# Optimization experiments

Measured on AMD Instinct MI355X. Metric: run time of the kernel, lower is better.

The kernel has to match this reference:

```python
import jax, jax.numpy as jnp
import numpy as np

N = 100000          # nodes
E = 1600000         # edges
KS = 3              # kernel_size per dim
DIM = 3             # pseudo-coordinate dim
CH = [1, 8, 16, 32, 16, 8, 1]
_BITS = ((0,0,0),(1,0,0),(0,1,0),(1,1,0),(0,0,1),(1,0,1),(0,1,1),(1,1,1))
_STRIDES = (1, KS, KS * KS)


def setup_inputs() -> dict:
    key = jax.random.key(0)
    ks = jax.random.split(key, 32)
    inp = {
        "x": jax.random.normal(ks[0], (N, 1), jnp.float32),
        "edge_index": jax.random.randint(ks[1], (2, E), 0, N),
        "pseudo": jax.random.uniform(ks[2], (E, DIM), dtype=jnp.float32),
    }
    ki = 3
    for i in range(6):
        fi, fo = CH[i], CH[i + 1]
        inp[f"w{i+1}"] = jax.random.normal(ks[ki], (KS**DIM, fi, fo), jnp.float32) / np.float32(np.sqrt(fi * 8)); ki += 1
        inp[f"root{i+1}"] = jax.random.normal(ks[ki], (fi, fo), jnp.float32) / np.float32(np.sqrt(fi)); ki += 1
        inp[f"b{i+1}"] = jnp.zeros((fo,), jnp.float32); ki += 1
    return inp


def spline_conv(x, src, dst, pseudo, W, root, bias):
    """Degree-1 open B-spline SplineConv, sum aggregation (norm=False) + root + bias.
    x: [N,Fin], pseudo: [E,DIM] in [0,1], W: [27,Fin,Fout]."""
    v = pseudo * (KS - 1)                              # [E,DIM] in [0,KS-1]
    f = jnp.clip(jnp.floor(v), 0.0, KS - 2)           # left knot per dim
    frac = v - f                                       # fractional part
    fi = f.astype(jnp.int32)
    # transform every node by all 27 kernel matrices once: [N,27,Fout]
    xw = jnp.einsum('nf,kfo->nko', x, W)
    m = jnp.zeros((src.shape[0], W.shape[-1]), x.dtype)
    for bits in _BITS:                                 # 2^DIM = 8 nonzero basis fns
        w = jnp.ones((src.shape[0],), x.dtype)
        idx = jnp.zeros((src.shape[0],), jnp.int32)
        for d in range(DIM):
            w = w * (frac[:, d] if bits[d] else (1.0 - frac[:, d]))
            idx = idx + (fi[:, d] + bits[d]) * _STRIDES[d]
        m = m + w[:, None] * xw[src, idx]              # gather [E,Fout]
    out = jax.ops.segment_sum(m, dst, num_segments=x.shape[0])
    return out + x @ root + bias


def reference(x, edge_index, pseudo, w1, root1, b1, w2, root2, b2, w3, root3, b3,
              w4, root4, b4, w5, root5, b5, w6, root6, b6):
    src, dst = edge_index[0], edge_index[1]
    h = x
    for (W, R, B) in ((w1, root1, b1), (w2, root2, b2), (w3, root3, b3),
                      (w4, root4, b4), (w5, root5, b5), (w6, root6, b6)):
        h = jax.nn.elu(spline_conv(h, src, dst, pseudo, W, R, B))
    return h.reshape(-1)
```

## Files before the change

kernel.cpp:

```cpp
#include <hip/hip_runtime.h>
#include <hip/hip_fp16.h>

#define N_NODES 100000
#define N_EDGES 1600000
#define TS      1024
#define NTILE   ((N_NODES + TS - 1) / TS)
#define NGRP    (NTILE * 8)
#define E_PAD2  (N_EDGES + NGRP * 64 + 256)
#define GRID_E2 (E_PAD2 / 256)

typedef _Float16 f16x8 __attribute__((ext_vector_type(8)));
typedef float    f32x4 __attribute__((ext_vector_type(4)));


__device__ __forceinline__ void pseudo_to_of(float p0, float p1, float p2,
                                             int& oct, float& fr0, float& fr1, float& fr2) {
    float v0 = p0 * 2.0f, v1 = p1 * 2.0f, v2 = p2 * 2.0f;
    int i0 = v0 >= 1.0f, i1 = v1 >= 1.0f, i2 = v2 >= 1.0f;
    fr0 = v0 - (float)i0; fr1 = v1 - (float)i1; fr2 = v2 - (float)i2;
    oct = i0 + 2 * i1 + 4 * i2;
}

template<int Fin>
__device__ __forceinline__ void loadx(const float* __restrict__ hp, float* x) {
    if constexpr (Fin % 4 == 0) {
        const float4* xv = reinterpret_cast<const float4*>(hp);
        #pragma unroll
        for (int f = 0; f < Fin / 4; ++f) {
            float4 t = xv[f];
            x[4*f+0] = t.x; x[4*f+1] = t.y; x[4*f+2] = t.z; x[4*f+3] = t.w;
        }
    } else {
        #pragma unroll
        for (int f = 0; f < Fin; ++f) x[f] = hp[f];
    }
}

template<int CH>
__device__ __forceinline__ void store_m_f16(__half* __restrict__ p, const float* z) {
    if constexpr (CH % 8 == 0) {
        #pragma unroll
        for (int q = 0; q < CH / 8; ++q) {
            union { uint4 v; __half2 h2[4]; } u;
            #pragma unroll
            for (int r = 0; r < 4; ++r)
                u.h2[r] = __floats2half2_rn(z[q*8 + 2*r], z[q*8 + 2*r + 1]);
            ((uint4*)p)[q] = u.v;
        }
    } else if constexpr (CH % 2 == 0) {
        #pragma unroll
        for (int q = 0; q < CH / 2; ++q)
            ((__half2*)p)[q] = __floats2half2_rn(z[2*q], z[2*q+1]);
    } else {
        #pragma unroll
        for (int o = 0; o < CH; ++o) p[o] = __float2half(z[o]);
    }
}

template<int CH>
__device__ __forceinline__ void accum_m_f16(float* acc, const __half* __restrict__ p) {
    if constexpr (CH % 8 == 0) {
        #pragma unroll
        for (int q = 0; q < CH / 8; ++q) {
            union { uint4 v; __half2 h2[4]; } u;
            u.v = ((const uint4*)p)[q];
            #pragma unroll
            for (int r = 0; r < 4; ++r) {
                float2 f = __half22float2(u.h2[r]);
                acc[q*8 + 2*r]     += f.x;
                acc[q*8 + 2*r + 1] += f.y;
            }
        }
    } else if constexpr (CH % 2 == 0) {
        #pragma unroll
        for (int q = 0; q < CH / 2; ++q) {
            float2 f = __half22float2(((const __half2*)p)[q]);
            acc[2*q] += f.x; acc[2*q+1] += f.y;
        }
    } else {
        #pragma unroll
        for (int o = 0; o < CH; ++o) acc[o] += __half2float(p[o]);
    }
}


__global__ __launch_bounds__(256) void count8_k(const int* __restrict__ dst,
                                                const float* __restrict__ pseudo,
                                                int* __restrict__ cnt8,
                                                unsigned short* __restrict__ rank16) {
    int e = blockIdx.x * 256 + threadIdx.x;
    if (e >= N_EDGES) return;
    int d = dst[e];
    size_t pb = (size_t)e * 3;
    int oct; float a, b, c;
    pseudo_to_of(pseudo[pb], pseudo[pb + 1], pseudo[pb + 2], oct, a, b, c);
    int r = atomicAdd(&cnt8[d * 8 + oct], 1);
    rank16[e] = (unsigned short)r;
}

__global__ __launch_bounds__(256) void scan_g1(const int* __restrict__ cnt8,
                                               int* __restrict__ gsum) {
    __shared__ int red[256];
    int g = blockIdx.x, t = threadIdx.x;
    int tile = g >> 3, oct = g & 7;
    int s = 0;
    #pragma unroll
    for (int q = 0; q < 4; ++q) {
        int n = tile * TS + t * 4 + q;
        if (n < N_NODES) s += cnt8[n * 8 + oct];
    }
    red[t] = s;
    __syncthreads();
    #pragma unroll
    for (int off = 128; off > 0; off >>= 1) {
        if (t < off) red[t] += red[t + off];
        __syncthreads();
    }
    if (t == 0) gsum[g] = red[0];
}

__global__ __launch_bounds__(1024) void scan_g2(const int* __restrict__ gsum,
                                                int* __restrict__ gbase,
                                                int* __restrict__ tot,
                                                unsigned char* __restrict__ winoct,
                                                uint4* __restrict__ slotmeta) {
    __shared__ int s[1024];
    __shared__ int sraw;
    int t = threadIdx.x;
    int v = 0;
    if (t < NGRP) v = ((gsum[t] + 63) >> 6) << 6;
    s[t] = v;
    __syncthreads();
    #pragma unroll
    for (int off = 1; off < 1024; off <<= 1) {
        int u = (t >= off) ? s[t - off] : 0;
        __syncthreads();
        s[t] += u;
        __syncthreads();
    }
    if (t < NGRP) gbase[t] = s[t] - v;
    if (t == NGRP - 1) sraw = s[t];
    __syncthreads();
    int raw = sraw;
    int totp = (raw + 255) & ~255;
    if (t == 0) { tot[0] = raw; tot[1] = totp; }
    int fill = totp - raw;
    if (t < fill) {
        uint4 z; z.x = z.y = z.z = z.w = 0u;
        slotmeta[raw + t] = z;
    }
    if (t < (fill >> 6)) winoct[(raw >> 6) + t] = 0;
}

__global__ __launch_bounds__(256) void scan_g3(const int* __restrict__ cnt8,
                                               const int* __restrict__ gbase,
                                               int* __restrict__ slotstart,
                                               unsigned char* __restrict__ winoct,
                                               uint4* __restrict__ slotmeta) {
    __shared__ int s[256];
    int g = blockIdx.x, t = threadIdx.x;
    int tile = g >> 3, oct = g & 7;
    int c[4];
    int sum = 0;
    #pragma unroll
    for (int q = 0; q < 4; ++q) {
        int n = tile * TS + t * 4 + q;
        c[q] = (n < N_NODES) ? cnt8[n * 8 + oct] : 0;
        sum += c[q];
    }
    s[t] = sum;
    __syncthreads();
    #pragma unroll
    for (int off = 1; off < 256; off <<= 1) {
        int u = (t >= off) ? s[t - off] : 0;
        __syncthreads();
        s[t] += u;
        __syncthreads();
    }
    int base = gbase[g];
    int run = base + s[t] - sum;
    #pragma unroll
    for (int q = 0; q < 4; ++q) {
        int n = tile * TS + t * 4 + q;
        if (n < N_NODES) { slotstart[n * 8 + oct] = run; run += c[q]; }
    }
    int cntg = s[255];
    int padded = ((cntg + 63) >> 6) << 6;
    for (int w = t; w < (padded >> 6); w += 256)
        winoct[(base >> 6) + w] = (unsigned char)oct;
    for (int i = t; i < padded - cntg; i += 256) {
        uint4 z; z.x = z.y = z.z = z.w = 0u;
        slotmeta[base + cntg + i] = z;
    }
}

__global__ __launch_bounds__(256) void scatter2_k(const int* __restrict__ src,
                                                  const int* __restrict__ dst,
                                                  const float* __restrict__ pseudo,
                                                  const unsigned short* __restrict__ rank16,
                                                  const int* __restrict__ slotstart,
                                                  uint4* __restrict__ slotmeta) {
    int e = blockIdx.x * 256 + threadIdx.x;
    if (e >= N_EDGES) return;
    int d = dst[e];
    size_t pb = (size_t)e * 3;
    int oct; float fr0, fr1, fr2;
    pseudo_to_of(pseudo[pb], pseudo[pb + 1], pseudo[pb + 2], oct, fr0, fr1, fr2);
    int slot = slotstart[d * 8 + oct] + (int)rank16[e];
    union { uint4 v; struct { int s; __half2 f01; __half2 f2x; unsigned pad; } t; } su;
    su.t.s   = src[e];
    su.t.f01 = __floats2half2_rn(fr0, fr1);
    su.t.f2x = __floats2half2_rn(fr2, 0.0f);
    su.t.pad = 0u;
    slotmeta[slot] = su.v;
}


template<int Fin, int Fout>
__global__ __launch_bounds__(256) void wprep_k(const float* __restrict__ W,
                                               _Float16* __restrict__ WB) {
    constexpr int K  = 8 * Fin;
    constexpr int KT = K / 32;
    constexpr int NT = (Fout + 15) / 16;
    const int total = 8 * KT * NT * 64 * 8;
    int i = blockIdx.x * 256 + threadIdx.x;
    if (i >= total) return;
    int j    = i & 7;
    int lane = (i >> 3) & 63;
    int rest = i >> 9;
    int nt = rest % NT; rest /= NT;
    int kt = rest % KT;
    int g  = rest / KT;
    int kb = lane >> 4, n = lane & 15;
    int k  = kt * 32 + kb * 8 + j;
    int b  = k / Fin, f = k % Fin;
    int bidx = (g & 1) + 3 * ((g >> 1) & 1) + 9 * ((g >> 2) & 1);
    int idx  = bidx + (b & 1) + 3 * ((b >> 1) & 1) + 9 * ((b >> 2) & 1);
    int col  = nt * 16 + n;
    float v = (col < Fout) ? W[((size_t)idx * Fin + f) * Fout + col] : 0.0f;
    WB[i] = (_Float16)v;
}


template<int Fin, int Fout>
__global__ __launch_bounds__(256) void msg_mfma_k(const float* __restrict__ h,
                                                  const uint4* __restrict__ slotmeta,
                                                  const unsigned char* __restrict__ winoct,
                                                  const int* __restrict__ tot,
                                                  const _Float16* __restrict__ WB,
                                                  __half* __restrict__ m) {
    constexpr int K  = 8 * Fin;
    constexpr int KT = K / 32;
    constexpr int NT = (Fout + 15) / 16;
    constexpr int LOG2FIN = (Fin == 8) ? 3 : (Fin == 16) ? 4 : 5;
    constexpr int XR = Fin;
    constexpr int ZR = NT * 16 + 8;

    __shared__ __align__(16) _Float16 xbuf[4][64 * XR];
    __shared__ __align__(16) _Float16 wbuf[4][64 * 8];
    __shared__ __align__(16) _Float16 zbuf[4][64 * ZR];

    const int base = blockIdx.x * 256;
    if (base >= tot[1]) return;

    const int tid = threadIdx.x, wv = tid >> 6, lane = tid & 63;
    const int slot = base + tid;

    int oct = winoct[(base >> 6) + wv];
    oct = __builtin_amdgcn_readfirstlane(oct);

    union { uint4 v; struct { int s; __half2 f01; __half2 f2x; unsigned pad; } t; } u;
    u.v = slotmeta[slot];
    int s = u.t.s;
    float2 f01 = __half22float2(u.t.f01);
    float2 f2x = __half22float2(u.t.f2x);
    float fr0 = f01.x, fr1 = f01.y, fr2 = f2x.x;
    float a0[2] = {1.0f - fr0, fr0};
    float a1[2] = {1.0f - fr1, fr1};
    float a2[2] = {1.0f - fr2, fr2};
    {
        union { uint4 v; __half2 h2[4]; } wu;
        #pragma unroll
        for (int q = 0; q < 4; ++q) {
            float wlo = a0[(2*q) & 1]     * a1[((2*q) >> 1) & 1]     * a2[((2*q) >> 2) & 1];
            float whi = a0[(2*q+1) & 1]   * a1[((2*q+1) >> 1) & 1]   * a2[((2*q+1) >> 2) & 1];
            wu.h2[q] = __floats2half2_rn(wlo, whi);
        }
        *((uint4*)&wbuf[wv][lane * 8]) = wu.v;
    }
    {
        float x[Fin];
        loadx<Fin>(h + (size_t)s * Fin, x);
        union { uint4 v[(Fin + 7) / 8]; __half2 h2[Fin / 2]; } xu;
        #pragma unroll
        for (int f = 0; f < Fin / 2; ++f)
            xu.h2[f] = __floats2half2_rn(x[2*f], x[2*f+1]);
        #pragma unroll
        for (int r = 0; r < Fin / 8; ++r)
            ((uint4*)&xbuf[wv][lane * XR])[r] = xu.v[r];
    }
    __syncthreads();

    f32x4 acc[4][NT];
    #pragma unroll
    for (int mt = 0; mt < 4; ++mt)
        #pragma unroll
        for (int nt = 0; nt < NT; ++nt)
            acc[mt][nt] = (f32x4){0.0f, 0.0f, 0.0f, 0.0f};

    const int kb = lane >> 4;
    const f16x8* __restrict__ WBv = (const f16x8*)WB;

    #pragma unroll
    for (int kt = 0; kt < KT; ++kt) {
        f16x8 bf[NT];
        #pragma unroll
        for (int nt = 0; nt < NT; ++nt)
            bf[nt] = WBv[((oct * KT + kt) * NT + nt) * 64 + lane];

        const int k0 = kt * 32 + kb * 8;
        const int b  = k0 >> LOG2FIN;
        const int f0 = k0 & (Fin - 1);

        #pragma unroll
        for (int mt = 0; mt < 4; ++mt) {
            const int e = mt * 16 + (lane & 15);
            f16x8 xa = *(const f16x8*)&xbuf[wv][e * XR + f0];
            _Float16 wh = wbuf[wv][e * 8 + b];
            f16x8 av;
            #pragma unroll
            for (int j = 0; j < 8; ++j) av[j] = xa[j] * wh;
            #pragma unroll
            for (int nt = 0; nt < NT; ++nt)
                acc[mt][nt] = __builtin_amdgcn_mfma_f32_16x16x32_f16(av, bf[nt], acc[mt][nt], 0, 0, 0);
        }
    }

    #pragma unroll
    for (int mt = 0; mt < 4; ++mt) {
        #pragma unroll
        for (int nt = 0; nt < NT; ++nt) {
            #pragma unroll
            for (int q = 0; q < 4; ++q) {
                int e = mt * 16 + (lane >> 4) * 4 + q;
                int o = nt * 16 + (lane & 15);
                zbuf[wv][e * ZR + o] = (_Float16)acc[mt][nt][q];
            }
        }
    }
    __syncthreads();

    constexpr int NV = (Fout * 2) / 16;
    const uint4* zr = (const uint4*)&zbuf[wv][lane * ZR];
    uint4* mp = (uint4*)(m + (size_t)slot * Fout);
    #pragma unroll
    for (int r = 0; r < NV; ++r) mp[r] = zr[r];
}


template<int Fin, int Fout, int CH>
__global__ __launch_bounds__(256) void msg_k(const float* __restrict__ h,
                                             const uint4* __restrict__ slotmeta,
                                             const unsigned char* __restrict__ winoct,
                                             const int* __restrict__ tot,
                                             const float* __restrict__ W,
                                             __half* __restrict__ m,
                                             int coff) {
    int base = blockIdx.x * 256;
    if (base >= tot[1]) return;
    int wv = threadIdx.x >> 6;
    int g = winoct[(base >> 6) + wv];
    g = __builtin_amdgcn_readfirstlane(g);
    const int bidx = (g & 1) + 3 * ((g >> 1) & 1) + 9 * ((g >> 2) & 1);

    int j = base + threadIdx.x;

    union { uint4 v; struct { int s; __half2 f01; __half2 f2x; unsigned pad; } t; } u;
    u.v = slotmeta[j];
    int s = u.t.s;
    float2 f01 = __half22float2(u.t.f01);
    float2 f2x = __half22float2(u.t.f2x);
    float fr0 = f01.x, fr1 = f01.y, fr2 = f2x.x;
    float a0[2] = {1.0f - fr0, fr0};
    float a1[2] = {1.0f - fr1, fr1};
    float a2[2] = {1.0f - fr2, fr2};
    float w[8];
    #pragma unroll
    for (int b = 0; b < 8; ++b)
        w[b] = a0[b & 1] * a1[(b >> 1) & 1] * a2[(b >> 2) & 1];

    float x[Fin];
    loadx<Fin>(h + (size_t)s * Fin, x);

    float z[CH];
    #pragma unroll
    for (int o = 0; o < CH; ++o) z[o] = 0.0f;

    #pragma unroll
    for (int b = 0; b < 8; ++b) {
        const int idx = bidx + (b & 1) + 3 * ((b >> 1) & 1) + 9 * ((b >> 2) & 1);
        const float* __restrict__ wp = W + (size_t)idx * (Fin * Fout) + coff;
        float wb = w[b];
        #pragma unroll
        for (int f = 0; f < Fin; ++f) {
            float a = wb * x[f];
            #pragma unroll
            for (int o = 0; o < CH; ++o) z[o] = fmaf(a, wp[f * Fout + o], z[o]);
        }
    }

    store_m_f16<CH>(m + (size_t)j * CH, z);
}


template<int Fin, int Fout, int CH>
__global__ __launch_bounds__(256) void gather_k(const float* __restrict__ hin,
                                                const __half* __restrict__ m,
                                                const int* __restrict__ slotstart,
                                                const int* __restrict__ cnt8,
                                                const float* __restrict__ root,
                                                const float* __restrict__ bias,
                                                float* __restrict__ hout,
                                                int coff) {
    int n = blockIdx.x * 256 + threadIdx.x;
    if (n >= N_NODES) return;

    float acc[CH];
    #pragma unroll
    for (int o = 0; o < CH; ++o) acc[o] = bias[coff + o];

    float x[Fin];
    loadx<Fin>(hin + (size_t)n * Fin, x);
    #pragma unroll
    for (int f = 0; f < Fin; ++f) {
        #pragma unroll
        for (int o = 0; o < CH; ++o)
            acc[o] = fmaf(x[f], root[f * Fout + coff + o], acc[o]);
    }

    int4 sa = ((const int4*)slotstart)[n * 2];
    int4 sb = ((const int4*)slotstart)[n * 2 + 1];
    int4 ca = ((const int4*)cnt8)[n * 2];
    int4 cb = ((const int4*)cnt8)[n * 2 + 1];
    int ss[8] = {sa.x, sa.y, sa.z, sa.w, sb.x, sb.y, sb.z, sb.w};
    int cc[8] = {ca.x, ca.y, ca.z, ca.w, cb.x, cb.y, cb.z, cb.w};

    #pragma unroll
    for (int oct = 0; oct < 8; ++oct) {
        int p = ss[oct];
        for (int j = 0; j < cc[oct]; ++j)
            accum_m_f16<CH>(acc, m + (size_t)(p + j) * CH);
    }

    #pragma unroll
    for (int o = 0; o < CH; ++o) {
        float t = acc[o];
        hout[(size_t)n * Fout + coff + o] = t > 0.0f ? t : expm1f(t);
    }
}


template<int Fin, int Fout>
__global__ __launch_bounds__(256) void init_out_k(const float* __restrict__ h,
                                                  const float* __restrict__ root,
                                                  const float* __restrict__ bias,
                                                  float* __restrict__ out) {
    int n = blockIdx.x * 256 + threadIdx.x;
    if (n >= N_NODES) return;
    float xr[Fin];
    #pragma unroll
    for (int f = 0; f < Fin; ++f) xr[f] = h[(size_t)n * Fin + f];
    float z[Fout];
    #pragma unroll
    for (int o = 0; o < Fout; ++o) z[o] = bias[o];
    #pragma unroll
    for (int f = 0; f < Fin; ++f)
        #pragma unroll
        for (int o = 0; o < Fout; ++o) z[o] += xr[f] * root[f * Fout + o];
    #pragma unroll
    for (int o = 0; o < Fout; ++o) out[(size_t)n * Fout + o] = z[o];
}

template<int Fin, int Fout>
__global__ __launch_bounds__(256) void edge_k(const float* __restrict__ h,
                                              const int* __restrict__ src,
                                              const int* __restrict__ dst,
                                              const float* __restrict__ pseudo,
                                              const float* __restrict__ W,
                                              float* __restrict__ out) {
    constexpr int KFF = Fin * Fout;
    constexpr int STRIDE = KFF + 1;
    __shared__ float sW[27 * STRIDE];
    for (int i = threadIdx.x; i < 27 * KFF; i += 256) {
        int k = i / KFF;
        sW[k * STRIDE + (i - k * KFF)] = W[i];
    }
    __syncthreads();
    int e = blockIdx.x * 256 + threadIdx.x;
    if (e >= N_EDGES) return;
    int s = src[e], d = dst[e];
    size_t pb = (size_t)e * 3;
    int oct; float fr0, fr1, fr2;
    pseudo_to_of(pseudo[pb], pseudo[pb+1], pseudo[pb+2], oct, fr0, fr1, fr2);
    int i0 = oct & 1, i1 = (oct >> 1) & 1, i2 = (oct >> 2) & 1;
    float a0[2] = {1.0f - fr0, fr0};
    float a1[2] = {1.0f - fr1, fr1};
    float a2[2] = {1.0f - fr2, fr2};
    float xr[Fin];
    #pragma unroll
    for (int f = 0; f < Fin; ++f) xr[f] = h[(size_t)s * Fin + f];
    float z[Fout];
    #pragma unroll
    for (int o = 0; o < Fout; ++o) z[o] = 0.0f;
    #pragma unroll
    for (int b = 0; b < 8; ++b) {
        int idx = (i0 + (b & 1)) + 3 * (i1 + ((b >> 1) & 1)) + 9 * (i2 + ((b >> 2) & 1));
        float wb = a0[b & 1] * a1[(b >> 1) & 1] * a2[(b >> 2) & 1];
        const float* wp = &sW[idx * STRIDE];
        #pragma unroll
        for (int f = 0; f < Fin; ++f) {
            float a = wb * xr[f];
            #pragma unroll
            for (int o = 0; o < Fout; ++o) z[o] += a * wp[f * Fout + o];
        }
    }
    float* op = out + (size_t)d * Fout;
    #pragma unroll
    for (int o = 0; o < Fout; ++o) atomicAdd(&op[o], z[o]);
}

__global__ __launch_bounds__(256) void elu_k(float* __restrict__ p, int total) {
    int i = blockIdx.x * 256 + threadIdx.x;
    if (i < total) {
        float t = p[i];
        p[i] = t > 0.0f ? t : expm1f(t);
    }
}


template<int Fin, int Fout>
static void run_layer_mfma(const float* hin, float* hout,
                           const float* W, const float* root, const float* bias,
                           const uint4* slotmeta, const unsigned char* winoct,
                           const int* tot, const int* slotstart, const int* cnt8,
                           _Float16* WB, __half* m, hipStream_t stream) {
    constexpr int K  = 8 * Fin;
    constexpr int KT = K / 32;
    constexpr int NT = (Fout + 15) / 16;
    const int wtotal = 8 * KT * NT * 64 * 8;
    wprep_k<Fin, Fout><<<(wtotal + 255) / 256, 256, 0, stream>>>(W, WB);
    msg_mfma_k<Fin, Fout><<<GRID_E2, 256, 0, stream>>>(hin, slotmeta, winoct, tot, WB, m);
    gather_k<Fin, Fout, Fout><<<(N_NODES + 255) / 256, 256, 0, stream>>>(
        hin, m, slotstart, cnt8, root, bias, hout, 0);
}

template<int Fin, int Fout>
static void run_layer_new(const float* hin, float* hout,
                          const float* W, const float* root, const float* bias,
                          const uint4* slotmeta, const unsigned char* winoct,
                          const int* tot, const int* slotstart, const int* cnt8,
                          __half* m, int chunk, hipStream_t stream) {
    const int GN = (N_NODES + 255) / 256;
    if (Fout <= chunk) {
        msg_k<Fin, Fout, Fout><<<GRID_E2, 256, 0, stream>>>(hin, slotmeta, winoct, tot, W, m, 0);
        gather_k<Fin, Fout, Fout><<<GN, 256, 0, stream>>>(hin, m, slotstart, cnt8, root, bias, hout, 0);
        return;
    }
    if constexpr (Fout > 16) {
        if (chunk == 16) {
            for (int p = 0; p < Fout / 16; ++p) {
                msg_k<Fin, Fout, 16><<<GRID_E2, 256, 0, stream>>>(hin, slotmeta, winoct, tot, W, m, 16 * p);
                gather_k<Fin, Fout, 16><<<GN, 256, 0, stream>>>(hin, m, slotstart, cnt8, root, bias, hout, 16 * p);
            }
            return;
        }
    }
    if constexpr (Fout > 8) {
        if (chunk == 8) {
            for (int p = 0; p < Fout / 8; ++p) {
                msg_k<Fin, Fout, 8><<<GRID_E2, 256, 0, stream>>>(hin, slotmeta, winoct, tot, W, m, 8 * p);
                gather_k<Fin, Fout, 8><<<GN, 256, 0, stream>>>(hin, m, slotstart, cnt8, root, bias, hout, 8 * p);
            }
            return;
        }
    }
    if constexpr (Fout > 4) {
        if (chunk == 4) {
            for (int p = 0; p < Fout / 4; ++p) {
                msg_k<Fin, Fout, 4><<<GRID_E2, 256, 0, stream>>>(hin, slotmeta, winoct, tot, W, m, 4 * p);
                gather_k<Fin, Fout, 4><<<GN, 256, 0, stream>>>(hin, m, slotstart, cnt8, root, bias, hout, 4 * p);
            }
            return;
        }
    }
    if constexpr (Fout > 2) {
        if (chunk == 2) {
            for (int p = 0; p < Fout / 2; ++p) {
                msg_k<Fin, Fout, 2><<<GRID_E2, 256, 0, stream>>>(hin, slotmeta, winoct, tot, W, m, 2 * p);
                gather_k<Fin, Fout, 2><<<GN, 256, 0, stream>>>(hin, m, slotstart, cnt8, root, bias, hout, 2 * p);
            }
            return;
        }
    }
}

template<int Fin, int Fout>
static void run_layer_old(const float* hin, float* hout,
                          const float* W, const float* root, const float* bias,
                          const int* src, const int* dst, const float* pseudo,
                          hipStream_t stream) {
    init_out_k<Fin, Fout><<<(N_NODES + 255) / 256, 256, 0, stream>>>(hin, root, bias, hout);
    edge_k<Fin, Fout><<<(N_EDGES + 255) / 256, 256, 0, stream>>>(hin, src, dst, pseudo, W, hout);
    int total = N_NODES * Fout;
    elu_k<<<(total + 255) / 256, 256, 0, stream>>>(hout, total);
}

extern "C" void kernel_launch(void* const* d_in, const int* in_sizes, int n_in,
                              void* d_out, int out_size, void* d_ws, size_t ws_size,
                              hipStream_t stream) {
    const float* x      = (const float*)d_in[0];
    const int*   ei     = (const int*)d_in[1];
    const float* pseudo = (const float*)d_in[2];
    const int* src = ei;
    const int* dst = ei + N_EDGES;

    const float* W[6]; const float* R[6]; const float* B[6];
    for (int i = 0; i < 6; ++i) {
        W[i] = (const float*)d_in[3 + 3 * i];
        R[i] = (const float*)d_in[4 + 3 * i];
        B[i] = (const float*)d_in[5 + 3 * i];
    }
    float* out = (float*)d_out;
    char* ws = (char*)d_ws;

    const int tiers[5] = {32, 16, 8, 4, 2};
    int chunk = 0;
    size_t o_hA = 0, o_hB = 0, o_c8 = 0, o_ss = 0, o_rk = 0, o_meta = 0,
           o_wo = 0, o_sm = 0, o_wb = 0, o_m = 0;
    for (int t = 0; t < 5; ++t) {
        int c = tiers[t];
        size_t off = 0;
        auto alloc = [&](size_t bytes) { size_t cur = off; off = (off + bytes + 255) & ~(size_t)255; return cur; };
        size_t a_hA   = alloc((size_t)N_NODES * 32 * 4);
        size_t a_hB   = alloc((size_t)N_NODES * 32 * 4);
        size_t a_c8   = alloc((size_t)N_NODES * 8 * 4);
        size_t a_ss   = alloc((size_t)N_NODES * 8 * 4);
        size_t a_rk   = alloc((size_t)N_EDGES * 2);
        size_t a_meta = alloc((size_t)(2 * NGRP + 8) * 4);
        size_t a_wo   = alloc((size_t)(E_PAD2 / 64));
        size_t a_sm   = alloc((size_t)E_PAD2 * 16);
        size_t a_wb   = alloc((size_t)4 * 65536 * 2);
        size_t a_m    = alloc((size_t)E_PAD2 * c * 2);
        if (off <= ws_size) {
            chunk = c;
            o_hA = a_hA; o_hB = a_hB; o_c8 = a_c8; o_ss = a_ss; o_rk = a_rk;
            o_meta = a_meta; o_wo = a_wo; o_sm = a_sm; o_wb = a_wb; o_m = a_m;
            break;
        }
    }

    if (chunk > 0) {
        float* hA      = (float*)(ws + o_hA);
        float* hB      = (float*)(ws + o_hB);
        int*   cnt8    = (int*)(ws + o_c8);
        int*   slotst  = (int*)(ws + o_ss);
        unsigned short* rank16 = (unsigned short*)(ws + o_rk);
        int*   gsum    = (int*)(ws + o_meta);
        int*   gbase   = gsum + NGRP;
        int*   tot     = gbase + NGRP;
        unsigned char* winoct = (unsigned char*)(ws + o_wo);
        uint4* slotmeta= (uint4*)(ws + o_sm);
        _Float16* WBb  = (_Float16*)(ws + o_wb);
        _Float16* WB2  = WBb;
        _Float16* WB3  = WBb + 65536;
        _Float16* WB4  = WBb + 2 * 65536;
        _Float16* WB5  = WBb + 3 * 65536;
        __half* m      = (__half*)(ws + o_m);

        hipMemsetAsync(cnt8, 0, (size_t)N_NODES * 8 * 4, stream);

        count8_k<<<N_EDGES / 256, 256, 0, stream>>>(dst, pseudo, cnt8, rank16);
        scan_g1<<<NGRP, 256, 0, stream>>>(cnt8, gsum);
        scan_g2<<<1, 1024, 0, stream>>>(gsum, gbase, tot, winoct, slotmeta);
        scan_g3<<<NGRP, 256, 0, stream>>>(cnt8, gbase, slotst, winoct, slotmeta);
        scatter2_k<<<N_EDGES / 256, 256, 0, stream>>>(src, dst, pseudo, rank16, slotst, slotmeta);

        run_layer_new<1, 8>(x, hA, W[0], R[0], B[0], slotmeta, winoct, tot, slotst, cnt8, m, chunk, stream);

        if (chunk == 32) {
            run_layer_mfma<8, 16> (hA, hB, W[1], R[1], B[1], slotmeta, winoct, tot, slotst, cnt8, WB2, m, stream);
            run_layer_mfma<16, 32>(hB, hA, W[2], R[2], B[2], slotmeta, winoct, tot, slotst, cnt8, WB3, m, stream);
            run_layer_mfma<32, 16>(hA, hB, W[3], R[3], B[3], slotmeta, winoct, tot, slotst, cnt8, WB4, m, stream);
            run_layer_mfma<16, 8> (hB, hA, W[4], R[4], B[4], slotmeta, winoct, tot, slotst, cnt8, WB5, m, stream);
        } else {
            run_layer_new<8, 16> (hA, hB, W[1], R[1], B[1], slotmeta, winoct, tot, slotst, cnt8, m, chunk, stream);
            run_layer_new<16, 32>(hB, hA, W[2], R[2], B[2], slotmeta, winoct, tot, slotst, cnt8, m, chunk, stream);
            run_layer_new<32, 16>(hA, hB, W[3], R[3], B[3], slotmeta, winoct, tot, slotst, cnt8, m, chunk, stream);
            run_layer_new<16, 8> (hB, hA, W[4], R[4], B[4], slotmeta, winoct, tot, slotst, cnt8, m, chunk, stream);
        }

        run_layer_new<8, 1>(hA, out, W[5], R[5], B[5], slotmeta, winoct, tot, slotst, cnt8, m, chunk, stream);
    } else {
        float* hA = (float*)ws;
        float* hB = hA + (size_t)N_NODES * 32;
        run_layer_old<1, 8>  (x,  hA, W[0], R[0], B[0], src, dst, pseudo, stream);
        run_layer_old<8, 16> (hA, hB, W[1], R[1], B[1], src, dst, pseudo, stream);
        run_layer_old<16, 32>(hB, hA, W[2], R[2], B[2], src, dst, pseudo, stream);
        run_layer_old<32, 16>(hA, hB, W[3], R[3], B[3], src, dst, pseudo, stream);
        run_layer_old<16, 8> (hB, hA, W[4], R[4], B[4], src, dst, pseudo, stream);
        run_layer_old<8, 1>  (hA, out, W[5], R[5], B[5], src, dst, pseudo, stream);
    }
}
```

Measured before the change: 453.0 us.

## Store hidden activations in fp16, gather features directly, and batch weight prep

Intermediate node features hA/hB are now stored as half precision, and the load/store helpers are templated to read and write either float or half. The MFMA message kernel drops its LDS staging of x and basis weights and the __syncthreads. Each lane instead loads its four edges' metadata, reads f16x8 features straight from global memory, and computes the trilinear basis weight inline. The four per-layer weight-prep launches are merged into one kernel issued up front. The aim is to halve activation memory traffic and cut launch and sync overhead, at the cost of extra rounding in the hidden layers and redundant global feature loads per k-tile.

```diff
diff --git a/kernel.cpp b/kernel.cpp
--- a/kernel.cpp
+++ b/kernel.cpp
@@ -22,7 +22,7 @@
 }
 
 template<int Fin>
-__device__ __forceinline__ void loadx(const float* __restrict__ hp, float* x) {
+__device__ __forceinline__ void loadanyT(const float* __restrict__ hp, float* x) {
     if constexpr (Fin % 4 == 0) {
         const float4* xv = reinterpret_cast<const float4*>(hp);
         #pragma unroll
@@ -36,8 +36,48 @@
     }
 }
 
+template<int Fin>
+__device__ __forceinline__ void loadanyT(const __half* __restrict__ hp, float* x) {
+    if constexpr (Fin % 8 == 0) {
+        #pragma unroll
+        for (int r = 0; r < Fin / 8; ++r) {
+            union { uint4 v; __half2 h2[4]; } u;
+            u.v = ((const uint4*)hp)[r];
+            #pragma unroll
+            for (int q = 0; q < 4; ++q) {
+                float2 f = __half22float2(u.h2[q]);
+                x[r*8 + 2*q]     = f.x;
+                x[r*8 + 2*q + 1] = f.y;
+            }
+        }
+    } else {
+        #pragma unroll
+        for (int f = 0; f < Fin; ++f) x[f] = __half2float(hp[f]);
+    }
+}
+
 template<int CH>
-__device__ __forceinline__ void store_m_f16(__half* __restrict__ p, const float* z) {
+__device__ __forceinline__ void storeanyT(float* __restrict__ p, const float* z) {
+    if constexpr (CH % 4 == 0) {
+        #pragma unroll
+        for (int o = 0; o < CH / 4; ++o) {
+            float4 t; t.x = z[4*o]; t.y = z[4*o+1]; t.z = z[4*o+2]; t.w = z[4*o+3];
+            ((float4*)p)[o] = t;
+        }
+    } else if constexpr (CH % 2 == 0) {
+        #pragma unroll
+        for (int o = 0; o < CH / 2; ++o) {
+            float2 t; t.x = z[2*o]; t.y = z[2*o+1];
+            ((float2*)p)[o] = t;
+        }
+    } else {
+        #pragma unroll
+        for (int o = 0; o < CH; ++o) p[o] = z[o];
+    }
+}
+
+template<int CH>
+__device__ __forceinline__ void storeanyT(__half* __restrict__ p, const float* z) {
     if constexpr (CH % 8 == 0) {
         #pragma unroll
         for (int q = 0; q < CH / 8; ++q) {
@@ -46,6 +86,14 @@
             for (int r = 0; r < 4; ++r)
                 u.h2[r] = __floats2half2_rn(z[q*8 + 2*r], z[q*8 + 2*r + 1]);
             ((uint4*)p)[q] = u.v;
+        }
+    } else if constexpr (CH % 4 == 0) {
+        #pragma unroll
+        for (int q = 0; q < CH / 4; ++q) {
+            union { uint2 v; __half2 h2[2]; } u;
+            u.h2[0] = __floats2half2_rn(z[4*q],     z[4*q + 1]);
+            u.h2[1] = __floats2half2_rn(z[4*q + 2], z[4*q + 3]);
+            ((uint2*)p)[q] = u.v;
         }
     } else if constexpr (CH % 2 == 0) {
         #pragma unroll
@@ -217,14 +265,10 @@
 
 
 template<int Fin, int Fout>
-__global__ __launch_bounds__(256) void wprep_k(const float* __restrict__ W,
-                                               _Float16* __restrict__ WB) {
-    constexpr int K  = 8 * Fin;
-    constexpr int KT = K / 32;
+__device__ __forceinline__ void wprep_elem(const float* __restrict__ W,
+                                           _Float16* __restrict__ WB, int i) {
+    constexpr int KT = (8 * Fin) / 32;
     constexpr int NT = (Fout + 15) / 16;
-    const int total = 8 * KT * NT * 64 * 8;
-    int i = blockIdx.x * 256 + threadIdx.x;
-    if (i >= total) return;
     int j    = i & 7;
     int lane = (i >> 3) & 63;
     int rest = i >> 9;
@@ -241,23 +285,42 @@
     WB[i] = (_Float16)v;
 }
 
+#define WS2 8192
+#define WS3 32768
+#define WS4 32768
+#define WS5 16384
+
+__global__ __launch_bounds__(256) void wprep_all_k(const float* __restrict__ W2,
+                                                   const float* __restrict__ W3,
+                                                   const float* __restrict__ W4,
+                                                   const float* __restrict__ W5,
+                                                   _Float16* __restrict__ WB2,
+                                                   _Float16* __restrict__ WB3,
+                                                   _Float16* __restrict__ WB4,
+                                                   _Float16* __restrict__ WB5) {
+    int i = blockIdx.x * 256 + threadIdx.x;
+    if (i < WS2) { wprep_elem<8, 16>(W2, WB2, i); return; }
+    i -= WS2;
+    if (i < WS3) { wprep_elem<16, 32>(W3, WB3, i); return; }
+    i -= WS3;
+    if (i < WS4) { wprep_elem<32, 16>(W4, WB4, i); return; }
+    i -= WS4;
+    if (i < WS5) { wprep_elem<16, 8>(W5, WB5, i); return; }
+}
+
 
 template<int Fin, int Fout>
-__global__ __launch_bounds__(256) void msg_mfma_k(const float* __restrict__ h,
+__global__ __launch_bounds__(256) void msg_mfma_k(const __half* __restrict__ h,
                                                   const uint4* __restrict__ slotmeta,
                                                   const unsigned char* __restrict__ winoct,
                                                   const int* __restrict__ tot,
                                                   const _Float16* __restrict__ WB,
                                                   __half* __restrict__ m) {
-    constexpr int K  = 8 * Fin;
-    constexpr int KT = K / 32;
+    constexpr int KT = (8 * Fin) / 32;
     constexpr int NT = (Fout + 15) / 16;
     constexpr int LOG2FIN = (Fin == 8) ? 3 : (Fin == 16) ? 4 : 5;
-    constexpr int XR = Fin;
     constexpr int ZR = NT * 16 + 8;
 
-    __shared__ __align__(16) _Float16 xbuf[4][64 * XR];
-    __shared__ __align__(16) _Float16 wbuf[4][64 * 8];
     __shared__ __align__(16) _Float16 zbuf[4][64 * ZR];
 
     const int base = blockIdx.x * 256;
@@ -265,41 +328,25 @@
 
     const int tid = threadIdx.x, wv = tid >> 6, lane = tid & 63;
     const int slot = base + tid;
+    const int wbase = base + wv * 64;
+    const int kb = lane >> 4;
 
     int oct = winoct[(base >> 6) + wv];
     oct = __builtin_amdgcn_readfirstlane(oct);
 
-    union { uint4 v; struct { int s; __half2 f01; __half2 f2x; unsigned pad; } t; } u;
-    u.v = slotmeta[slot];
-    int s = u.t.s;
-    float2 f01 = __half22float2(u.t.f01);
-    float2 f2x = __half22float2(u.t.f2x);
-    float fr0 = f01.x, fr1 = f01.y, fr2 = f2x.x;
-    float a0[2] = {1.0f - fr0, fr0};
-    float a1[2] = {1.0f - fr1, fr1};
-    float a2[2] = {1.0f - fr2, fr2};
-    {
-        union { uint4 v; __half2 h2[4]; } wu;
-        #pragma unroll
-        for (int q = 0; q < 4; ++q) {
-            float wlo = a0[(2*q) & 1]     * a1[((2*q) >> 1) & 1]     * a2[((2*q) >> 2) & 1];
-            float whi = a0[(2*q+1) & 1]   * a1[((2*q+1) >> 1) & 1]   * a2[((2*q+1) >> 2) & 1];
-            wu.h2[q] = __floats2half2_rn(wlo, whi);
-        }
-        *((uint4*)&wbuf[wv][lane * 8]) = wu.v;
-    }
-    {
-        float x[Fin];
-        loadx<Fin>(h + (size_t)s * Fin, x);
-        union { uint4 v[(Fin + 7) / 8]; __half2 h2[Fin / 2]; } xu;
-        #pragma unroll
-        for (int f = 0; f < Fin / 2; ++f)
-            xu.h2[f] = __floats2half2_rn(x[2*f], x[2*f+1]);
-        #pragma unroll
-        for (int r = 0; r < Fin / 8; ++r)
-            ((uint4*)&xbuf[wv][lane * XR])[r] = xu.v[r];
-    }
-    __syncthreads();
+    int   sE[4];
+    float g0[4], h0[4], g1[4], h1[4], g2[4], h2v[4];
+    #pragma unroll
+    for (int mt = 0; mt < 4; ++mt) {
+        union { uint4 v; struct { int s; __half2 f01; __half2 f2x; unsigned pad; } t; } u;
+        u.v = slotmeta[wbase + mt * 16 + (lane & 15)];
+        sE[mt] = u.t.s;
+        float2 f01 = __half22float2(u.t.f01);
+        float2 f2x = __half22float2(u.t.f2x);
+        g0[mt] = 1.0f - f01.x; h0[mt] = f01.x;
+        g1[mt] = 1.0f - f01.y; h1[mt] = f01.y;
+        g2[mt] = 1.0f - f2x.x; h2v[mt] = f2x.x;
+    }
 
     f32x4 acc[4][NT];
     #pragma unroll
@@ -308,8 +355,8 @@
         for (int nt = 0; nt < NT; ++nt)
             acc[mt][nt] = (f32x4){0.0f, 0.0f, 0.0f, 0.0f};
 
-    const int kb = lane >> 4;
     const f16x8* __restrict__ WBv = (const f16x8*)WB;
+    const f16x8* __restrict__ hv  = (const f16x8*)h;
 
     #pragma unroll
     for (int kt = 0; kt < KT; ++kt) {
@@ -320,13 +367,15 @@
 
         const int k0 = kt * 32 + kb * 8;
         const int b  = k0 >> LOG2FIN;
-        const int f0 = k0 & (Fin - 1);
+        const int f8 = (k0 & (Fin - 1)) >> 3;
 
         #pragma unroll
         for (int mt = 0; mt < 4; ++mt) {
-            const int e = mt * 16 + (lane & 15);
-            f16x8 xa = *(const f16x8*)&xbuf[wv][e * XR + f0];
-            _Float16 wh = wbuf[wv][e * 8 + b];
+            f16x8 xa = hv[(size_t)sE[mt] * (Fin / 8) + f8];
+            float w = ((b & 1) ? h0[mt] : g0[mt])
+                    * ((b & 2) ? h1[mt] : g1[mt])
+                    * ((b & 4) ? h2v[mt] : g2[mt]);
+            _Float16 wh = (_Float16)w;
             f16x8 av;
             #pragma unroll
             for (int j = 0; j < 8; ++j) av[j] = xa[j] * wh;
@@ -358,8 +407,8 @@
 }
 
 
-template<int Fin, int Fout, int CH>
-__global__ __launch_bounds__(256) void msg_k(const float* __restrict__ h,
+template<int Fin, int Fout, int CH, typename TIn>
+__global__ __launch_bounds__(256) void msg_k(const TIn* __restrict__ h,
                                              const uint4* __restrict__ slotmeta,
                                              const unsigned char* __restrict__ winoct,
                                              const int* __restrict__ tot,
@@ -390,7 +439,7 @@
         w[b] = a0[b & 1] * a1[(b >> 1) & 1] * a2[(b >> 2) & 1];
 
     float x[Fin];
-    loadx<Fin>(h + (size_t)s * Fin, x);
+    loadanyT<Fin>(h + (size_t)s * Fin, x);
 
     float z[CH];
     #pragma unroll
@@ -409,18 +458,18 @@
         }
     }
 
-    store_m_f16<CH>(m + (size_t)j * CH, z);
-}
-
-
-template<int Fin, int Fout, int CH>
-__global__ __launch_bounds__(256) void gather_k(const float* __restrict__ hin,
+    storeanyT<CH>(m + (size_t)j * CH, z);
+}
+
+
+template<int Fin, int Fout, int CH, typename TIn, typename TOut>
+__global__ __launch_bounds__(256) void gather_k(const TIn* __restrict__ hin,
                                                 const __half* __restrict__ m,
                                                 const int* __restrict__ slotstart,
                                                 const int* __restrict__ cnt8,
                                                 const float* __restrict__ root,
                                                 const float* __restrict__ bias,
-                                                float* __restrict__ hout,
+                                                TOut* __restrict__ hout,
                                                 int coff) {
     int n = blockIdx.x * 256 + threadIdx.x;
     if (n >= N_NODES) return;
@@ -430,7 +479,7 @@
     for (int o = 0; o < CH; ++o) acc[o] = bias[coff + o];
 
     float x[Fin];
-    loadx<Fin>(hin + (size_t)n * Fin, x);
+    loadanyT<Fin>(hin + (size_t)n * Fin, x);
     #pragma unroll
     for (int f = 0; f < Fin; ++f) {
         #pragma unroll
@@ -452,11 +501,13 @@
             accum_m_f16<CH>(acc, m + (size_t)(p + j) * CH);
     }
 
+    float zz[CH];
     #pragma unroll
     for (int o = 0; o < CH; ++o) {
         float t = acc[o];
-        hout[(size_t)n * Fout + coff + o] = t > 0.0f ? t : expm1f(t);
-    }
+        zz[o] = t > 0.0f ? t : expm1f(t);
+    }
+    storeanyT<CH>(hout + (size_t)n * Fout + coff, zz);
 }
 
 
@@ -538,39 +589,34 @@
 }
 
 
-template<int Fin, int Fout>
-static void run_layer_mfma(const float* hin, float* hout,
+template<int Fin, int Fout, typename TIn, typename TOut>
+static void run_layer_mfma(const TIn* hin, TOut* hout,
+                           const float* root, const float* bias,
+                           const uint4* slotmeta, const unsigned char* winoct,
+                           const int* tot, const int* slotstart, const int* cnt8,
+                           const _Float16* WB, __half* m, hipStream_t stream) {
+    msg_mfma_k<Fin, Fout><<<GRID_E2, 256, 0, stream>>>(hin, slotmeta, winoct, tot, WB, m);
+    gather_k<Fin, Fout, Fout, TIn, TOut><<<(N_NODES + 255) / 256, 256, 0, stream>>>(
+        hin, m, slotstart, cnt8, root, bias, hout, 0);
+}
+
+template<int Fin, int Fout, typename TIn, typename TOut>
+static void run_layer_valu(const TIn* hin, TOut* hout,
                            const float* W, const float* root, const float* bias,
                            const uint4* slotmeta, const unsigned char* winoct,
                            const int* tot, const int* slotstart, const int* cnt8,
-                           _Float16* WB, __half* m, hipStream_t stream) {
-    constexpr int K  = 8 * Fin;
-    constexpr int KT = K / 32;
-    constexpr int NT = (Fout + 15) / 16;
-    const int wtotal = 8 * KT * NT * 64 * 8;
-    wprep_k<Fin, Fout><<<(wtotal + 255) / 256, 256, 0, stream>>>(W, WB);
-    msg_mfma_k<Fin, Fout><<<GRID_E2, 256, 0, stream>>>(hin, slotmeta, winoct, tot, WB, m);
-    gather_k<Fin, Fout, Fout><<<(N_NODES + 255) / 256, 256, 0, stream>>>(
-        hin, m, slotstart, cnt8, root, bias, hout, 0);
-}
-
-template<int Fin, int Fout>
-static void run_layer_new(const float* hin, float* hout,
-                          const float* W, const float* root, const float* bias,
-                          const uint4* slotmeta, const unsigned char* winoct,
-                          const int* tot, const int* slotstart, const int* cnt8,
-                          __half* m, int chunk, hipStream_t stream) {
+                           __half* m, int chunk, hipStream_t stream) {
     const int GN = (N_NODES + 255) / 256;
     if (Fout <= chunk) {
-        msg_k<Fin, Fout, Fout><<<GRID_E2, 256, 0, stream>>>(hin, slotmeta, winoct, tot, W, m, 0);
-        gather_k<Fin, Fout, Fout><<<GN, 256, 0, stream>>>(hin, m, slotstart, cnt8, root, bias, hout, 0);
+        msg_k<Fin, Fout, Fout, TIn><<<GRID_E2, 256, 0, stream>>>(hin, slotmeta, winoct, tot, W, m, 0);
+        gather_k<Fin, Fout, Fout, TIn, TOut><<<GN, 256, 0, stream>>>(hin, m, slotstart, cnt8, root, bias, hout, 0);
         return;
     }
     if constexpr (Fout > 16) {
         if (chunk == 16) {
             for (int p = 0; p < Fout / 16; ++p) {
-                msg_k<Fin, Fout, 16><<<GRID_E2, 256, 0, stream>>>(hin, slotmeta, winoct, tot, W, m, 16 * p);
-                gather_k<Fin, Fout, 16><<<GN, 256, 0, stream>>>(hin, m, slotstart, cnt8, root, bias, hout, 16 * p);
+                msg_k<Fin, Fout, 16, TIn><<<GRID_E2, 256, 0, stream>>>(hin, slotmeta, winoct, tot, W, m, 16 * p);
+                gather_k<Fin, Fout, 16, TIn, TOut><<<GN, 256, 0, stream>>>(hin, m, slotstart, cnt8, root, bias, hout, 16 * p);
             }
             return;
         }
@@ -578,8 +624,8 @@
     if constexpr (Fout > 8) {
         if (chunk == 8) {
             for (int p = 0; p < Fout / 8; ++p) {
-                msg_k<Fin, Fout, 8><<<GRID_E2, 256, 0, stream>>>(hin, slotmeta, winoct, tot, W, m, 8 * p);
-                gather_k<Fin, Fout, 8><<<GN, 256, 0, stream>>>(hin, m, slotstart, cnt8, root, bias, hout, 8 * p);
+                msg_k<Fin, Fout, 8, TIn><<<GRID_E2, 256, 0, stream>>>(hin, slotmeta, winoct, tot, W, m, 8 * p);
+                gather_k<Fin, Fout, 8, TIn, TOut><<<GN, 256, 0, stream>>>(hin, m, slotstart, cnt8, root, bias, hout, 8 * p);
             }
             return;
         }
@@ -587,8 +633,8 @@
     if constexpr (Fout > 4) {
         if (chunk == 4) {
             for (int p = 0; p < Fout / 4; ++p) {
-                msg_k<Fin, Fout, 4><<<GRID_E2, 256, 0, stream>>>(hin, slotmeta, winoct, tot, W, m, 4 * p);
-                gather_k<Fin, Fout, 4><<<GN, 256, 0, stream>>>(hin, m, slotstart, cnt8, root, bias, hout, 4 * p);
+                msg_k<Fin, Fout, 4, TIn><<<GRID_E2, 256, 0, stream>>>(hin, slotmeta, winoct, tot, W, m, 4 * p);
+                gather_k<Fin, Fout, 4, TIn, TOut><<<GN, 256, 0, stream>>>(hin, m, slotstart, cnt8, root, bias, hout, 4 * p);
             }
             return;
         }
@@ -596,8 +642,8 @@
     if constexpr (Fout > 2) {
         if (chunk == 2) {
             for (int p = 0; p < Fout / 2; ++p) {
-                msg_k<Fin, Fout, 2><<<GRID_E2, 256, 0, stream>>>(hin, slotmeta, winoct, tot, W, m, 2 * p);
-                gather_k<Fin, Fout, 2><<<GN, 256, 0, stream>>>(hin, m, slotstart, cnt8, root, bias, hout, 2 * p);
+                msg_k<Fin, Fout, 2, TIn><<<GRID_E2, 256, 0, stream>>>(hin, slotmeta, winoct, tot, W, m, 2 * p);
+                gather_k<Fin, Fout, 2, TIn, TOut><<<GN, 256, 0, stream>>>(hin, m, slotstart, cnt8, root, bias, hout, 2 * p);
             }
             return;
         }
@@ -641,8 +687,8 @@
         int c = tiers[t];
         size_t off = 0;
         auto alloc = [&](size_t bytes) { size_t cur = off; off = (off + bytes + 255) & ~(size_t)255; return cur; };
-        size_t a_hA   = alloc((size_t)N_NODES * 32 * 4);
-        size_t a_hB   = alloc((size_t)N_NODES * 32 * 4);
+        size_t a_hA   = alloc((size_t)N_NODES * 32 * 2);
+        size_t a_hB   = alloc((size_t)N_NODES * 32 * 2);
         size_t a_c8   = alloc((size_t)N_NODES * 8 * 4);
         size_t a_ss   = alloc((size_t)N_NODES * 8 * 4);
         size_t a_rk   = alloc((size_t)N_EDGES * 2);
@@ -660,8 +706,8 @@
     }
 
     if (chunk > 0) {
-        float* hA      = (float*)(ws + o_hA);
-        float* hB      = (float*)(ws + o_hB);
+        __half* hA     = (__half*)(ws + o_hA);
+        __half* hB     = (__half*)(ws + o_hB);
         int*   cnt8    = (int*)(ws + o_c8);
         int*   slotst  = (int*)(ws + o_ss);
         unsigned short* rank16 = (unsigned short*)(ws + o_rk);
@@ -685,29 +731,44 @@
         scan_g3<<<NGRP, 256, 0, stream>>>(cnt8, gbase, slotst, winoct, slotmeta);
         scatter2_k<<<N_EDGES / 256, 256, 0, stream>>>(src, dst, pseudo, rank16, slotst, slotmeta);
 
-        run_layer_new<1, 8>(x, hA, W[0], R[0], B[0], slotmeta, winoct, tot, slotst, cnt8, m, chunk, stream);
-
         if (chunk == 32) {
-            run_layer_mfma<8, 16> (hA, hB, W[1], R[1], B[1], slotmeta, winoct, tot, slotst, cnt8, WB2, m, stream);
-            run_layer_mfma<16, 32>(hB, hA, W[2], R[2], B[2], slotmeta, winoct, tot, slotst, cnt8, WB3, m, stream);
-            run_layer_mfma<32, 16>(hA, hB, W[3], R[3], B[3], slotmeta, winoct, tot, slotst, cnt8, WB4, m, stream);
-            run_layer_mfma<16, 8> (hB, hA, W[4], R[4], B[4], slotmeta, winoct, tot, slotst, cnt8, WB5, m, stream);
+            wprep_all_k<<<(WS2 + WS3 + WS4 + WS5 + 255) / 256, 256, 0, stream>>>(
+                W[1], W[2], W[3], W[4], WB2, WB3, WB4, WB5);
+
+            run_layer_valu<1, 8, float, __half>(x, hA, W[0], R[0], B[0], slotmeta, winoct, tot,
+                                                slotst, cnt8, m, chunk, stream);
+            run_layer_mfma<8, 16, __half, __half>(hA, hB, R[1], B[1], slotmeta, winoct, tot,
+                                                  slotst, cnt8, WB3 - 65536, m, stream);
+            run_layer_mfma<16, 32, __half, __half>(hB, hA, R[2], B[2], slotmeta, winoct, tot,
+                                                   slotst, cnt8, WB3, m, stream);
+            run_layer_mfma<32, 16, __half, __half>(hA, hB, R[3], B[3], slotmeta, winoct, tot,
+                                                   slotst, cnt8, WB4, m, stream);
+            run_layer_mfma<16, 8, __half, __half>(hB, hA, R[4], B[4], slotmeta, winoct, tot,
+                                                  slotst, cnt8, WB5, m, stream);
+            run_layer_valu<8, 1, __half, float>(hA, out, W[5], R[5], B[5], slotmeta, winoct, tot,
+                                                slotst, cnt8, m, chunk, stream);
         } else {
-            run_layer_new<8, 16> (hA, hB, W[1], R[1], B[1], slotmeta, winoct, tot, slotst, cnt8, m, chunk, stream);
-            run_layer_new<16, 32>(hB, hA, W[2], R[2], B[2], slotmeta, winoct, tot, slotst, cnt8, m, chunk, stream);
-            run_layer_new<32, 16>(hA, hB, W[3], R[3], B[3], slotmeta, winoct, tot, slotst, cnt8, m, chunk, stream);
-            run_layer_new<16, 8> (hB, hA, W[4], R[4], B[4], slotmeta, winoct, tot, slotst, cnt8, m, chunk, stream);
-        }
-
-        run_layer_new<8, 1>(hA, out, W[5], R[5], B[5], slotmeta, winoct, tot, slotst, cnt8, m, chunk, stream);
+            run_layer_valu<1, 8, float, __half>(x, hA, W[0], R[0], B[0], slotmeta, winoct, tot,
+                                                slotst, cnt8, m, chunk, stream);
+            run_layer_valu<8, 16, __half, __half>(hA, hB, W[1], R[1], B[1], slotmeta, winoct, tot,
+                                                  slotst, cnt8, m, chunk, stream);
+            run_layer_valu<16, 32, __half, __half>(hB, hA, W[2], R[2], B[2], slotmeta, winoct, tot,
+                                                   slotst, cnt8, m, chunk, stream);
+            run_layer_valu<32, 16, __half, __half>(hA, hB, W[3], R[3], B[3], slotmeta, winoct, tot,
+                                                   slotst, cnt8, m, chunk, stream);
+            run_layer_valu<16, 8, __half, __half>(hB, hA, W[4], R[4], B[4], slotmeta, winoct, tot,
+                                                  slotst, cnt8, m, chunk, stream);
+            run_layer_valu<8, 1, __half, float>(hA, out, W[5], R[5], B[5], slotmeta, winoct, tot,
+                                                slotst, cnt8, m, chunk, stream);
+        }
     } else {
-        float* hA = (float*)ws;
-        float* hB = hA + (size_t)N_NODES * 32;
-        run_layer_old<1, 8>  (x,  hA, W[0], R[0], B[0], src, dst, pseudo, stream);
-        run_layer_old<8, 16> (hA, hB, W[1], R[1], B[1], src, dst, pseudo, stream);
-        run_layer_old<16, 32>(hB, hA, W[2], R[2], B[2], src, dst, pseudo, stream);
-        run_layer_old<32, 16>(hA, hB, W[3], R[3], B[3], src, dst, pseudo, stream);
-        run_layer_old<16, 8> (hB, hA, W[4], R[4], B[4], src, dst, pseudo, stream);
-        run_layer_old<8, 1>  (hA, out, W[5], R[5], B[5], src, dst, pseudo, stream);
-    }
-}
+        float* hAf = (float*)ws;
+        float* hBf = hAf + (size_t)N_NODES * 32;
+        run_layer_old<1, 8>  (x,   hAf, W[0], R[0], B[0], src, dst, pseudo, stream);
+        run_layer_old<8, 16> (hAf, hBf, W[1], R[1], B[1], src, dst, pseudo, stream);
+        run_layer_old<16, 32>(hBf, hAf, W[2], R[2], B[2], src, dst, pseudo, stream);
+        run_layer_old<32, 16>(hAf, hBf, W[3], R[3], B[3], src, dst, pseudo, stream);
+        run_layer_old<16, 8> (hBf, hAf, W[4], R[4], B[4], src, dst, pseudo, stream);
+        run_layer_old<8, 1>  (hAf, out, W[5], R[5], B[5], src, dst, pseudo, stream);
+    }
+}
```

Result: faster. 403.4 us (-10.9%).
